# Kernel optimization log

Measured on AMD Instinct MI355X. Metric: run time of the kernel, lower is better.

Reference implementation:

```python
import jax, jax.numpy as jnp
import numpy as np

HEADS, HEAD_DIM = 8, 32
FOLD_W = FOLD_H = 8
PW = PH = 2  # proposal_w/h -> M = PW*PH centers per region


def setup_inputs() -> dict:
    key = jax.random.key(0)
    ks = jax.random.split(key, 8)
    dim, hd = 96, HEADS * HEAD_DIM
    return {
        "x": jax.random.normal(ks[0], (16, dim, 64, 64), jnp.float32),
        "Wf": jax.random.normal(ks[1], (hd, dim), jnp.float32) * 0.05,
        "bf": jax.random.normal(ks[2], (hd,), jnp.float32) * 0.01,
        "Wv": jax.random.normal(ks[3], (hd, dim), jnp.float32) * 0.05,
        "bv": jax.random.normal(ks[4], (hd,), jnp.float32) * 0.01,
        "Wp": jax.random.normal(ks[5], (dim, hd), jnp.float32) * 0.05,
        "bp": jax.random.normal(ks[6], (dim,), jnp.float32) * 0.01,
        "sim_alpha": jnp.ones((1,), jnp.float32),
        "sim_beta": jnp.zeros((1,), jnp.float32),
    }


def _l2norm(t):
    # matches torch F.normalize(dim=-1, eps=1e-12)
    n = jnp.maximum(jnp.linalg.norm(t, axis=-1, keepdims=True), 1e-12)
    return t / n


def _cluster_forward(x, Wf, bf, Wv, bv, Wp, bp, sim_alpha, sim_beta):
    B, C, W, H = x.shape
    # 1x1 convs
    v = jnp.einsum("bchw,oc->bohw", x, Wv) + bv[None, :, None, None]
    f = jnp.einsum("bchw,oc->bohw", x, Wf) + bf[None, :, None, None]

    def split_heads(t):  # b (e c) w h -> (b e) c w h
        b = t.shape[0]
        return t.reshape(b, HEADS, HEAD_DIM, W, H).reshape(b * HEADS, HEAD_DIM, W, H)

    f, v = split_heads(f), split_heads(v)

    def fold(t):  # b c (f1 w) (f2 h) -> (b f1 f2) c w h
        b, c, w0, h0 = t.shape
        ws, hs = w0 // FOLD_W, h0 // FOLD_H
        t = t.reshape(b, c, FOLD_W, ws, FOLD_H, hs)
        return t.transpose(0, 2, 4, 1, 3, 5).reshape(b * FOLD_W * FOLD_H, c, ws, hs)

    f, v = fold(f), fold(v)
    b, c, w, h = f.shape

    def pool(t):  # AdaptiveMaxPool2d((PW,PH)); divides evenly -> block max
        return t.reshape(b, c, PW, w // PW, PH, h // PH).max(axis=(3, 5))

    centers = pool(f).reshape(b, c, PW * PH).transpose(0, 2, 1)       # [b,M,c]
    value_centers = pool(v).reshape(b, c, PW * PH).transpose(0, 2, 1)  # [b,M,c]
    pts = f.reshape(b, c, w * h).transpose(0, 2, 1)                    # [b,N,c]

    cos = jnp.einsum("bmc,bnc->bmn", _l2norm(centers), _l2norm(pts))
    sim = jax.nn.sigmoid(sim_beta + sim_alpha * cos)                   # [b,M,N]

    # hard assignment: each point keeps only its best center
    idx = jnp.argmax(sim, axis=1)                                      # [b,N]
    mask = jax.nn.one_hot(idx, sim.shape[1], dtype=sim.dtype)          # [b,N,M]
    mask = jnp.transpose(mask, (0, 2, 1))                              # [b,M,N]
    sim = sim * mask

    value2 = v.reshape(b, c, w * h).transpose(0, 2, 1)                 # [b,N,c]
    # gather points -> centers
    agg = (jnp.einsum("bnc,bmn->bmc", value2, sim) + value_centers) / (
        mask.sum(axis=-1, keepdims=True) + 1.0
    )
    # dispatch centers -> points
    out = jnp.einsum("bmc,bmn->bnc", agg, sim)                         # [b,N,c]
    out = out.transpose(0, 2, 1).reshape(b, c, w, h)

    # unfold regions back
    bb = b // (FOLD_W * FOLD_H)
    out = out.reshape(bb, FOLD_W, FOLD_H, c, w, h).transpose(0, 3, 1, 4, 2, 5)
    out = out.reshape(bb, c, FOLD_W * w, FOLD_H * h)
    # merge heads: (b e) c w h -> b (e c) w h
    out = out.reshape(bb // HEADS, HEADS * HEAD_DIM, W, H)
    out = jnp.einsum("bchw,oc->bohw", out, Wp) + bp[None, :, None, None]
    return out


def reference(x, Wf, bf, Wv, bv, Wp, bp, sim_alpha, sim_beta):
    return _cluster_forward(x, Wf, bf, Wv, bv, Wp, bp, sim_alpha, sim_beta)
```

## Files before the change

kernel.cpp:

```cpp
#include <hip/hip_runtime.h>
#include <math.h>


#define TPB 256

__global__ __launch_bounds__(TPB, 4)
void cc_main(const float* __restrict__ x,
             const float* __restrict__ Wf, const float* __restrict__ bf,
             const float* __restrict__ Wv, const float* __restrict__ bv,
             const float* __restrict__ salpha, const float* __restrict__ sbeta,
             float* __restrict__ disp)
{
    __shared__ __align__(16) float smem[8320];
    __shared__ float cfs[2][132], cvs[2][132], swb[2][256], aggs[2][132];

    const int t    = threadIdx.x;
    const int lane = t & 63;
    const int wid  = __builtin_amdgcn_readfirstlane(t >> 6);
    const int tc   = t >> 4;
    const int tp   = t & 15;
    const int blk  = blockIdx.x;
    const int f1   = blk & 7;
    const int f2   = (blk >> 3) & 7;
    const int heg  = (blk >> 6) & 3;
    const int bb   = blk >> 8;
    const int fold = f1*8 + f2;

    const float* xb = x + (size_t)bb*96*4096 + (size_t)(f1*8)*64 + f2*8;

    float acc[8][4];
    {
        const float* bsrc = (tc < 8) ? (bf + heg*64 + tc*8)
                                     : (bv + heg*64 + (tc-8)*8);
        float4 b0 = *(const float4*)bsrc;
        float4 b1 = *(const float4*)(bsrc + 4);
        #pragma unroll
        for (int i = 0; i < 4; ++i) {
            acc[0][i]=b0.x; acc[1][i]=b0.y; acc[2][i]=b0.z; acc[3][i]=b0.w;
            acc[4][i]=b1.x; acc[5][i]=b1.y; acc[6][i]=b1.z; acc[7][i]=b1.w;
        }
    }

    int xoff[2], xdst[2];
    #pragma unroll
    for (int i = 0; i < 2; ++i) {
        int fl = i*256 + t;
        int kl = fl >> 4, sg = fl & 15;
        xoff[i] = kl*4096 + (sg >> 1)*64 + (sg & 1)*4;
        xdst[i] = 4096 + kl*64 + sg*4;
    }
    int wdst[4];
    const float* wptr[4];
    #pragma unroll
    for (int i = 0; i < 4; ++i) {
        int fl = i*256 + t;
        int rr = fl & 127, kq = fl >> 7;
        wptr[i] = ((rr < 64) ? (Wf + (size_t)(heg*64 + rr)*96)
                             : (Wv + (size_t)(heg*64 + rr - 64)*96)) + kq*4;
        wdst[i] = (kq*4)*128 + rr;
    }

    float4 pxr[2], pwr[4];
    #pragma unroll
    for (int i = 0; i < 2; ++i) pxr[i] = *(const float4*)(xb + xoff[i]);
    #pragma unroll
    for (int i = 0; i < 4; ++i) pwr[i] = *(const float4*)(wptr[i]);
    #pragma unroll
    for (int i = 0; i < 2; ++i) *(float4*)&smem[xdst[i]] = pxr[i];
    #pragma unroll
    for (int i = 0; i < 4; ++i) {
        smem[wdst[i]      ] = pwr[i].x;
        smem[wdst[i] + 128] = pwr[i].y;
        smem[wdst[i] + 256] = pwr[i].z;
        smem[wdst[i] + 384] = pwr[i].w;
    }
    __syncthreads();

    for (int kc = 0; ; ) {
        if (kc < 64) {
            #pragma unroll
            for (int i = 0; i < 2; ++i)
                pxr[i] = *(const float4*)(xb + (kc+32)*4096 + xoff[i]);
            #pragma unroll
            for (int i = 0; i < 4; ++i)
                pwr[i] = *(const float4*)(wptr[i] + kc + 32);
        }
        #pragma unroll 4
        for (int k = 0; k < 32; ++k) {
            float4 wa  = *(const float4*)&smem[k*128 + tc*8];
            float4 wb4 = *(const float4*)&smem[k*128 + tc*8 + 4];
            float4 xq  = *(const float4*)&smem[4096 + k*64 + tp*4];
            float xv[4] = {xq.x, xq.y, xq.z, xq.w};
            #pragma unroll
            for (int i = 0; i < 4; ++i) {
                acc[0][i] = fmaf(wa.x,  xv[i], acc[0][i]);
                acc[1][i] = fmaf(wa.y,  xv[i], acc[1][i]);
                acc[2][i] = fmaf(wa.z,  xv[i], acc[2][i]);
                acc[3][i] = fmaf(wa.w,  xv[i], acc[3][i]);
                acc[4][i] = fmaf(wb4.x, xv[i], acc[4][i]);
                acc[5][i] = fmaf(wb4.y, xv[i], acc[5][i]);
                acc[6][i] = fmaf(wb4.z, xv[i], acc[6][i]);
                acc[7][i] = fmaf(wb4.w, xv[i], acc[7][i]);
            }
        }
        if (kc == 64) break;
        __syncthreads();
        #pragma unroll
        for (int i = 0; i < 2; ++i) *(float4*)&smem[xdst[i]] = pxr[i];
        #pragma unroll
        for (int i = 0; i < 4; ++i) {
            smem[wdst[i]      ] = pwr[i].x;
            smem[wdst[i] + 128] = pwr[i].y;
            smem[wdst[i] + 256] = pwr[i].z;
            smem[wdst[i] + 384] = pwr[i].w;
        }
        __syncthreads();
        kc += 32;
    }

    const float alpha = salpha[0], beta = sbeta[0];
    __syncthreads();
    #pragma unroll
    for (int j = 0; j < 8; ++j)
        #pragma unroll
        for (int i2 = 0; i2 < 4; ++i2)
            smem[(tc*8 + j)*65 + tp*4 + i2] = acc[j][i2];
    __syncthreads();

    if (wid < 2) {
        const int he = wid, slot = he;
        {
            int m = lane >> 4, c0 = (lane & 15)*2;
            int pw = m >> 1, ph = m & 1;
            #pragma unroll
            for (int cc = 0; cc < 2; ++cc) {
                int c = c0 + cc;
                float mf = -3.402823466e38f, mv = -3.402823466e38f;
                #pragma unroll
                for (int a = 0; a < 4; ++a)
                    #pragma unroll
                    for (int b2 = 0; b2 < 4; ++b2) {
                        int n = (pw*4 + a)*8 + ph*4 + b2;
                        mf = fmaxf(mf, smem[(he*32 + c)*65 + n]);
                        mv = fmaxf(mv, smem[(64 + he*32 + c)*65 + n]);
                    }
                cfs[slot][m*33 + c] = mf;
                cvs[slot][m*33 + c] = mv;
            }
        }
        float d0=0,d1=0,d2=0,d3=0,pn=0,cn0=0,cn1=0,cn2=0,cn3=0;
        #pragma unroll 8
        for (int c = 0; c < 32; ++c) {
            float fv = smem[(he*32 + c)*65 + lane];
            float m0 = cfs[slot][c], m1 = cfs[slot][33+c];
            float m2 = cfs[slot][66+c], m3 = cfs[slot][99+c];
            d0 = fmaf(m0, fv, d0); d1 = fmaf(m1, fv, d1);
            d2 = fmaf(m2, fv, d2); d3 = fmaf(m3, fv, d3);
            pn = fmaf(fv, fv, pn);
            cn0 = fmaf(m0, m0, cn0); cn1 = fmaf(m1, m1, cn1);
            cn2 = fmaf(m2, m2, cn2); cn3 = fmaf(m3, m3, cn3);
        }
        float ip = 1.f / fmaxf(sqrtf(pn), 1e-12f);
        float z0 = beta + alpha*(d0*(1.f/fmaxf(sqrtf(cn0),1e-12f))*ip);
        float z1 = beta + alpha*(d1*(1.f/fmaxf(sqrtf(cn1),1e-12f))*ip);
        float z2 = beta + alpha*(d2*(1.f/fmaxf(sqrtf(cn2),1e-12f))*ip);
        float z3 = beta + alpha*(d3*(1.f/fmaxf(sqrtf(cn3),1e-12f))*ip);
        float s0 = 1.f/(1.f + expf(-z0));
        float s1 = 1.f/(1.f + expf(-z1));
        float s2 = 1.f/(1.f + expf(-z2));
        float s3 = 1.f/(1.f + expf(-z3));
        int bi = 0; float bvv = s0;
        if (s1 > bvv) { bvv = s1; bi = 1; }
        if (s2 > bvv) { bvv = s2; bi = 2; }
        if (s3 > bvv) { bvv = s3; bi = 3; }
        int cnt0 = __popcll(__ballot(bi == 0));
        int cnt1 = __popcll(__ballot(bi == 1));
        int cnt2 = __popcll(__ballot(bi == 2));
        int cnt3 = __popcll(__ballot(bi == 3));
        swb[slot][lane]       = (bi==0) ? bvv : 0.f;
        swb[slot][64 + lane]  = (bi==1) ? bvv : 0.f;
        swb[slot][128 + lane] = (bi==2) ? bvv : 0.f;
        swb[slot][192 + lane] = (bi==3) ? bvv : 0.f;
        #pragma unroll
        for (int it = 0; it < 2; ++it) {
            int m = it*2 + (lane >> 5);
            int c = lane & 31;
            float s = 0.f;
            #pragma unroll 8
            for (int n2 = 0; n2 < 64; ++n2)
                s = fmaf(smem[(64 + he*32 + c)*65 + n2],
                         swb[slot][m*64 + n2], s);
            int cm = (m==0) ? cnt0 : (m==1) ? cnt1 : (m==2) ? cnt2 : cnt3;
            aggs[slot][m*33 + c] = (s + cvs[slot][m*33 + c]) / (float)(cm + 1);
        }
        const int e32 = (heg*2 + he)*32;
        const size_t obase = (size_t)bb*4096 + (size_t)fold*64 + lane;
        #pragma unroll 4
        for (int c = 0; c < 32; ++c)
            disp[(size_t)(e32 + c)*65536 + obase] = aggs[slot][bi*33 + c] * bvv;
    }
}

__global__ __launch_bounds__(TPB, 8)
void cc_proj(const float* __restrict__ disp, const float* __restrict__ Wp,
             const float* __restrict__ bp, float* __restrict__ out)
{
    __shared__ __align__(16) float wch[3200];
    __shared__ __align__(16) float xch[1024];
    const int t   = threadIdx.x;
    const int toc = t >> 4;
    const int tp  = t & 15;
    const int blk = blockIdx.x;
    const int f1   = blk & 7;
    const int half = (blk >> 3) & 1;
    const int f2   = (blk >> 4) & 7;
    const int bb   = blk >> 7;
    const int fold = f1*8 + f2;
    const int pxbase = bb*4096 + fold*64 + half*32;

    float acc[6][2];
    #pragma unroll
    for (int o = 0; o < 6; ++o) {
        float b = bp[toc*6 + o];
        acc[o][0] = b; acc[o][1] = b;
    }

    int woffg[3], wdst[3];
    #pragma unroll
    for (int i = 0; i < 3; ++i) {
        int fl = i*256 + t;
        int oc2 = fl % 96, kq = fl / 96;
        woffg[i] = oc2*256 + kq*4;
        wdst[i]  = (kq*4)*100 + oc2;
    }
    const int xoffg = (t >> 3)*65536 + pxbase + (t & 7)*4;
    const int xdst  = (t >> 3)*32 + (t & 7)*4;

    float4 pwr[3], pxr;
    #pragma unroll
    for (int i = 0; i < 3; ++i) pwr[i] = *(const float4*)(Wp + woffg[i]);
    pxr = *(const float4*)(disp + xoffg);
    #pragma unroll
    for (int i = 0; i < 3; ++i) {
        wch[wdst[i]      ] = pwr[i].x; wch[wdst[i] + 100] = pwr[i].y;
        wch[wdst[i] + 200] = pwr[i].z; wch[wdst[i] + 300] = pwr[i].w;
    }
    *(float4*)&xch[xdst] = pxr;
    __syncthreads();

    for (int kc = 0; ; ) {
        if (kc < 224) {
            #pragma unroll
            for (int i = 0; i < 3; ++i)
                pwr[i] = *(const float4*)(Wp + woffg[i] + kc + 32);
            pxr = *(const float4*)(disp + xoffg + (size_t)(kc+32)*65536);
        }
        #pragma unroll 4
        for (int k = 0; k < 32; ++k) {
            float2 wA = *(const float2*)&wch[k*100 + toc*6];
            float2 wB = *(const float2*)&wch[k*100 + toc*6 + 2];
            float2 wC = *(const float2*)&wch[k*100 + toc*6 + 4];
            float2 xv = *(const float2*)&xch[k*32 + tp*2];
            acc[0][0] = fmaf(wA.x, xv.x, acc[0][0]);
            acc[0][1] = fmaf(wA.x, xv.y, acc[0][1]);
            acc[1][0] = fmaf(wA.y, xv.x, acc[1][0]);
            acc[1][1] = fmaf(wA.y, xv.y, acc[1][1]);
            acc[2][0] = fmaf(wB.x, xv.x, acc[2][0]);
            acc[2][1] = fmaf(wB.x, xv.y, acc[2][1]);
            acc[3][0] = fmaf(wB.y, xv.x, acc[3][0]);
            acc[3][1] = fmaf(wB.y, xv.y, acc[3][1]);
            acc[4][0] = fmaf(wC.x, xv.x, acc[4][0]);
            acc[4][1] = fmaf(wC.x, xv.y, acc[4][1]);
            acc[5][0] = fmaf(wC.y, xv.x, acc[5][0]);
            acc[5][1] = fmaf(wC.y, xv.y, acc[5][1]);
        }
        if (kc == 224) break;
        __syncthreads();
        #pragma unroll
        for (int i = 0; i < 3; ++i) {
            wch[wdst[i]      ] = pwr[i].x; wch[wdst[i] + 100] = pwr[i].y;
            wch[wdst[i] + 200] = pwr[i].z; wch[wdst[i] + 300] = pwr[i].w;
        }
        *(float4*)&xch[xdst] = pxr;
        __syncthreads();
        kc += 32;
    }

    const int n = half*32 + tp*2;
    const int r = n >> 3, hh = n & 7;
    size_t oaddr = (size_t)bb*96*4096 + (size_t)(toc*6)*4096
                 + (size_t)(f1*8 + r)*64 + f2*8 + hh;
    #pragma unroll
    for (int o = 0; o < 6; ++o) {
        float2 st; st.x = acc[o][0]; st.y = acc[o][1];
        *(float2*)&out[oaddr + (size_t)o*4096] = st;
    }
}

extern "C" void kernel_launch(void* const* d_in, const int* in_sizes, int n_in,
                              void* d_out, int out_size, void* d_ws, size_t ws_size,
                              hipStream_t stream) {
    (void)in_sizes; (void)n_in; (void)out_size; (void)ws_size;
    float* disp = (float*)d_ws;
    cc_main<<<dim3(4096), dim3(TPB), 0, stream>>>(
        (const float*)d_in[0],
        (const float*)d_in[1],
        (const float*)d_in[2],
        (const float*)d_in[3],
        (const float*)d_in[4],
        (const float*)d_in[7],
        (const float*)d_in[8],
        disp);
    cc_proj<<<dim3(2048), dim3(TPB), 0, stream>>>(
        disp,
        (const float*)d_in[5],
        (const float*)d_in[6],
        (float*)d_out);
}
```

Measured before the change: 260.0 us.

## Map waves to channels and pixels to lanes; read weights as uniform scalars

Both kernels are restructured so each wave owns a group of 32 (or 24) output channels and each lane owns one pixel, accumulating all channels in registers. Weights are read directly from global memory with wave-uniform addresses, which can become scalar loads, instead of being staged in LDS. The pooling max is done with DPP and a shuffle across lanes rather than through an LDS round trip. The feature projections stay in registers for the cosine step, and the projection kernel launches half as many blocks. This cuts LDS traffic and barriers, at the cost of higher register pressure and scalar-load latency.

Measured after the change: 272.1 us. 4.7% more time.

```diff
diff --git a/kernel.cpp b/kernel.cpp
--- a/kernel.cpp
+++ b/kernel.cpp
@@ -3,6 +3,13 @@
 
 
 #define TPB 256
+
+template<int CTRL>
+__device__ __forceinline__ float dpp_max(float v) {
+    int s = __builtin_bit_cast(int, v);
+    int p = __builtin_amdgcn_update_dpp(0, s, CTRL, 0xF, 0xF, true);
+    return fmaxf(v, __builtin_bit_cast(float, p));
+}
 
 __global__ __launch_bounds__(TPB, 4)
 void cc_main(const float* __restrict__ x,
@@ -11,14 +18,19 @@
              const float* __restrict__ salpha, const float* __restrict__ sbeta,
              float* __restrict__ disp)
 {
-    __shared__ __align__(16) float smem[8320];
-    __shared__ float cfs[2][132], cvs[2][132], swb[2][256], aggs[2][132];
+    __shared__ __align__(16) float xch[64*33];
+    __shared__ __align__(16) float vd[2][64*33];
+    __shared__ __align__(16) float cfs[2][128];
+    __shared__ __align__(16) float cvs[2][128];
+    __shared__ float swb[2][256];
+    __shared__ float2 bib[2][64];
+    __shared__ float cnts[2][4];
+    __shared__ float aggs[2][132];
 
     const int t    = threadIdx.x;
     const int lane = t & 63;
     const int wid  = __builtin_amdgcn_readfirstlane(t >> 6);
-    const int tc   = t >> 4;
-    const int tp   = t & 15;
+    const int he   = wid & 1;
     const int blk  = blockIdx.x;
     const int f1   = blk & 7;
     const int f2   = (blk >> 3) & 7;
@@ -28,137 +40,85 @@
 
     const float* xb = x + (size_t)bb*96*4096 + (size_t)(f1*8)*64 + f2*8;
 
-    float acc[8][4];
-    {
-        const float* bsrc = (tc < 8) ? (bf + heg*64 + tc*8)
-                                     : (bv + heg*64 + (tc-8)*8);
-        float4 b0 = *(const float4*)bsrc;
-        float4 b1 = *(const float4*)(bsrc + 4);
-        #pragma unroll
-        for (int i = 0; i < 4; ++i) {
-            acc[0][i]=b0.x; acc[1][i]=b0.y; acc[2][i]=b0.z; acc[3][i]=b0.w;
-            acc[4][i]=b1.x; acc[5][i]=b1.y; acc[6][i]=b1.z; acc[7][i]=b1.w;
-        }
-    }
-
-    int xoff[2], xdst[2];
+    const float* wrow = (wid < 2) ? (Wf + (size_t)(heg*64 + wid*32)*96)
+                                  : (Wv + (size_t)(heg*64 + (wid-2)*32)*96);
+    const float* brow = (wid < 2) ? (bf + heg*64 + wid*32)
+                                  : (bv + heg*64 + (wid-2)*32);
+
+    float acc[32];
+    #pragma unroll
+    for (int c = 0; c < 32; ++c) acc[c] = brow[c];
+
+    int xoff[2], xbs[2];
     #pragma unroll
     for (int i = 0; i < 2; ++i) {
         int fl = i*256 + t;
         int kl = fl >> 4, sg = fl & 15;
         xoff[i] = kl*4096 + (sg >> 1)*64 + (sg & 1)*4;
-        xdst[i] = 4096 + kl*64 + sg*4;
-    }
-    int wdst[4];
-    const float* wptr[4];
-    #pragma unroll
-    for (int i = 0; i < 4; ++i) {
-        int fl = i*256 + t;
-        int rr = fl & 127, kq = fl >> 7;
-        wptr[i] = ((rr < 64) ? (Wf + (size_t)(heg*64 + rr)*96)
-                             : (Wv + (size_t)(heg*64 + rr - 64)*96)) + kq*4;
-        wdst[i] = (kq*4)*128 + rr;
-    }
-
-    float4 pxr[2], pwr[4];
-    #pragma unroll
-    for (int i = 0; i < 2; ++i) pxr[i] = *(const float4*)(xb + xoff[i]);
-    #pragma unroll
-    for (int i = 0; i < 4; ++i) pwr[i] = *(const float4*)(wptr[i]);
-    #pragma unroll
-    for (int i = 0; i < 2; ++i) *(float4*)&smem[xdst[i]] = pxr[i];
-    #pragma unroll
-    for (int i = 0; i < 4; ++i) {
-        smem[wdst[i]      ] = pwr[i].x;
-        smem[wdst[i] + 128] = pwr[i].y;
-        smem[wdst[i] + 256] = pwr[i].z;
-        smem[wdst[i] + 384] = pwr[i].w;
-    }
+        xbs[i]  = ((sg >> 1)*8 + (sg & 1)*4)*33 + kl;
+    }
+
+    float4 pxr0 = *(const float4*)(xb + xoff[0]);
+    float4 pxr1 = *(const float4*)(xb + xoff[1]);
+    xch[xbs[0]] = pxr0.x; xch[xbs[0]+33] = pxr0.y;
+    xch[xbs[0]+66] = pxr0.z; xch[xbs[0]+99] = pxr0.w;
+    xch[xbs[1]] = pxr1.x; xch[xbs[1]+33] = pxr1.y;
+    xch[xbs[1]+66] = pxr1.z; xch[xbs[1]+99] = pxr1.w;
     __syncthreads();
 
+    const int lx = lane*33;
     for (int kc = 0; ; ) {
         if (kc < 64) {
-            #pragma unroll
-            for (int i = 0; i < 2; ++i)
-                pxr[i] = *(const float4*)(xb + (kc+32)*4096 + xoff[i]);
-            #pragma unroll
-            for (int i = 0; i < 4; ++i)
-                pwr[i] = *(const float4*)(wptr[i] + kc + 32);
-        }
-        #pragma unroll 4
-        for (int k = 0; k < 32; ++k) {
-            float4 wa  = *(const float4*)&smem[k*128 + tc*8];
-            float4 wb4 = *(const float4*)&smem[k*128 + tc*8 + 4];
-            float4 xq  = *(const float4*)&smem[4096 + k*64 + tp*4];
-            float xv[4] = {xq.x, xq.y, xq.z, xq.w};
-            #pragma unroll
-            for (int i = 0; i < 4; ++i) {
-                acc[0][i] = fmaf(wa.x,  xv[i], acc[0][i]);
-                acc[1][i] = fmaf(wa.y,  xv[i], acc[1][i]);
-                acc[2][i] = fmaf(wa.z,  xv[i], acc[2][i]);
-                acc[3][i] = fmaf(wa.w,  xv[i], acc[3][i]);
-                acc[4][i] = fmaf(wb4.x, xv[i], acc[4][i]);
-                acc[5][i] = fmaf(wb4.y, xv[i], acc[5][i]);
-                acc[6][i] = fmaf(wb4.z, xv[i], acc[6][i]);
-                acc[7][i] = fmaf(wb4.w, xv[i], acc[7][i]);
+            pxr0 = *(const float4*)(xb + (kc+32)*4096 + xoff[0]);
+            pxr1 = *(const float4*)(xb + (kc+32)*4096 + xoff[1]);
+        }
+        #pragma unroll
+        for (int kg = 0; kg < 4; ++kg) {
+            float xv[8];
+            #pragma unroll
+            for (int j = 0; j < 8; ++j) xv[j] = xch[lx + kg*8 + j];
+            #pragma unroll
+            for (int c = 0; c < 32; ++c) {
+                const float* wp = wrow + c*96 + (kc + kg*8);
+                #pragma unroll
+                for (int j = 0; j < 8; ++j)
+                    acc[c] = fmaf(wp[j], xv[j], acc[c]);
             }
         }
         if (kc == 64) break;
         __syncthreads();
-        #pragma unroll
-        for (int i = 0; i < 2; ++i) *(float4*)&smem[xdst[i]] = pxr[i];
-        #pragma unroll
-        for (int i = 0; i < 4; ++i) {
-            smem[wdst[i]      ] = pwr[i].x;
-            smem[wdst[i] + 128] = pwr[i].y;
-            smem[wdst[i] + 256] = pwr[i].z;
-            smem[wdst[i] + 384] = pwr[i].w;
-        }
+        xch[xbs[0]] = pxr0.x; xch[xbs[0]+33] = pxr0.y;
+        xch[xbs[0]+66] = pxr0.z; xch[xbs[0]+99] = pxr0.w;
+        xch[xbs[1]] = pxr1.x; xch[xbs[1]+33] = pxr1.y;
+        xch[xbs[1]+66] = pxr1.z; xch[xbs[1]+99] = pxr1.w;
         __syncthreads();
         kc += 32;
     }
 
     const float alpha = salpha[0], beta = sbeta[0];
-    __syncthreads();
-    #pragma unroll
-    for (int j = 0; j < 8; ++j)
-        #pragma unroll
-        for (int i2 = 0; i2 < 4; ++i2)
-            smem[(tc*8 + j)*65 + tp*4 + i2] = acc[j][i2];
-    __syncthreads();
+    const int m = ((lane >> 5) & 1)*2 + ((lane >> 2) & 1);
+    const bool rep = (lane & 27) == 0;
+    #pragma unroll
+    for (int c = 0; c < 32; ++c) {
+        float rm = acc[c];
+        rm = dpp_max<0xB1>(rm);
+        rm = dpp_max<0x4E>(rm);
+        rm = dpp_max<0x128>(rm);
+        rm = fmaxf(rm, __shfl_xor(rm, 16));
+        if (rep) { if (wid < 2) cfs[he][c*4 + m] = rm; else cvs[he][c*4 + m] = rm; }
+    }
 
     if (wid < 2) {
-        const int he = wid, slot = he;
-        {
-            int m = lane >> 4, c0 = (lane & 15)*2;
-            int pw = m >> 1, ph = m & 1;
-            #pragma unroll
-            for (int cc = 0; cc < 2; ++cc) {
-                int c = c0 + cc;
-                float mf = -3.402823466e38f, mv = -3.402823466e38f;
-                #pragma unroll
-                for (int a = 0; a < 4; ++a)
-                    #pragma unroll
-                    for (int b2 = 0; b2 < 4; ++b2) {
-                        int n = (pw*4 + a)*8 + ph*4 + b2;
-                        mf = fmaxf(mf, smem[(he*32 + c)*65 + n]);
-                        mv = fmaxf(mv, smem[(64 + he*32 + c)*65 + n]);
-                    }
-                cfs[slot][m*33 + c] = mf;
-                cvs[slot][m*33 + c] = mv;
-            }
-        }
         float d0=0,d1=0,d2=0,d3=0,pn=0,cn0=0,cn1=0,cn2=0,cn3=0;
-        #pragma unroll 8
+        #pragma unroll
         for (int c = 0; c < 32; ++c) {
-            float fv = smem[(he*32 + c)*65 + lane];
-            float m0 = cfs[slot][c], m1 = cfs[slot][33+c];
-            float m2 = cfs[slot][66+c], m3 = cfs[slot][99+c];
-            d0 = fmaf(m0, fv, d0); d1 = fmaf(m1, fv, d1);
-            d2 = fmaf(m2, fv, d2); d3 = fmaf(m3, fv, d3);
+            float4 cf = *(const float4*)&cfs[he][c*4];
+            float fv = acc[c];
+            d0 = fmaf(cf.x, fv, d0); d1 = fmaf(cf.y, fv, d1);
+            d2 = fmaf(cf.z, fv, d2); d3 = fmaf(cf.w, fv, d3);
             pn = fmaf(fv, fv, pn);
-            cn0 = fmaf(m0, m0, cn0); cn1 = fmaf(m1, m1, cn1);
-            cn2 = fmaf(m2, m2, cn2); cn3 = fmaf(m3, m3, cn3);
+            cn0 = fmaf(cf.x, cf.x, cn0); cn1 = fmaf(cf.y, cf.y, cn1);
+            cn2 = fmaf(cf.z, cf.z, cn2); cn3 = fmaf(cf.w, cf.w, cn3);
         }
         float ip = 1.f / fmaxf(sqrtf(pn), 1e-12f);
         float z0 = beta + alpha*(d0*(1.f/fmaxf(sqrtf(cn0),1e-12f))*ip);
@@ -177,124 +137,113 @@
         int cnt1 = __popcll(__ballot(bi == 1));
         int cnt2 = __popcll(__ballot(bi == 2));
         int cnt3 = __popcll(__ballot(bi == 3));
-        swb[slot][lane]       = (bi==0) ? bvv : 0.f;
-        swb[slot][64 + lane]  = (bi==1) ? bvv : 0.f;
-        swb[slot][128 + lane] = (bi==2) ? bvv : 0.f;
-        swb[slot][192 + lane] = (bi==3) ? bvv : 0.f;
+        swb[he][lane]       = (bi==0) ? bvv : 0.f;
+        swb[he][64 + lane]  = (bi==1) ? bvv : 0.f;
+        swb[he][128 + lane] = (bi==2) ? bvv : 0.f;
+        swb[he][192 + lane] = (bi==3) ? bvv : 0.f;
+        bib[he][lane] = make_float2(bvv, (float)bi);
+        if (lane == 0) {
+            cnts[he][0] = (float)cnt0; cnts[he][1] = (float)cnt1;
+            cnts[he][2] = (float)cnt2; cnts[he][3] = (float)cnt3;
+        }
+    } else {
+        #pragma unroll
+        for (int c = 0; c < 32; ++c) vd[he][lane*33 + c] = acc[c];
+    }
+    __syncthreads();
+
+    if (wid >= 2) {
+        const int cI = lane & 31;
         #pragma unroll
         for (int it = 0; it < 2; ++it) {
-            int m = it*2 + (lane >> 5);
-            int c = lane & 31;
+            int mm = it*2 + (lane >> 5);
             float s = 0.f;
             #pragma unroll 8
             for (int n2 = 0; n2 < 64; ++n2)
-                s = fmaf(smem[(64 + he*32 + c)*65 + n2],
-                         swb[slot][m*64 + n2], s);
-            int cm = (m==0) ? cnt0 : (m==1) ? cnt1 : (m==2) ? cnt2 : cnt3;
-            aggs[slot][m*33 + c] = (s + cvs[slot][m*33 + c]) / (float)(cm + 1);
-        }
+                s = fmaf(vd[he][n2*33 + cI], swb[he][mm*64 + n2], s);
+            aggs[he][mm*33 + cI] = (s + cvs[he][cI*4 + mm]) / (cnts[he][mm] + 1.f);
+        }
+        float2 b2 = bib[he][lane];
+        float bvv = b2.x; int bi = (int)b2.y;
         const int e32 = (heg*2 + he)*32;
         const size_t obase = (size_t)bb*4096 + (size_t)fold*64 + lane;
         #pragma unroll 4
         for (int c = 0; c < 32; ++c)
-            disp[(size_t)(e32 + c)*65536 + obase] = aggs[slot][bi*33 + c] * bvv;
-    }
-}
-
-__global__ __launch_bounds__(TPB, 8)
+            disp[(size_t)(e32 + c)*65536 + obase] = aggs[he][bi*33 + c] * bvv;
+    }
+}
+
+__global__ __launch_bounds__(TPB, 4)
 void cc_proj(const float* __restrict__ disp, const float* __restrict__ Wp,
              const float* __restrict__ bp, float* __restrict__ out)
 {
-    __shared__ __align__(16) float wch[3200];
-    __shared__ __align__(16) float xch[1024];
-    const int t   = threadIdx.x;
-    const int toc = t >> 4;
-    const int tp  = t & 15;
-    const int blk = blockIdx.x;
+    __shared__ __align__(16) float xch[64*33];
+    const int t    = threadIdx.x;
+    const int lane = t & 63;
+    const int wid  = __builtin_amdgcn_readfirstlane(t >> 6);
+    const int blk  = blockIdx.x;
     const int f1   = blk & 7;
-    const int half = (blk >> 3) & 1;
-    const int f2   = (blk >> 4) & 7;
-    const int bb   = blk >> 7;
+    const int f2   = (blk >> 3) & 7;
+    const int bb   = blk >> 6;
     const int fold = f1*8 + f2;
-    const int pxbase = bb*4096 + fold*64 + half*32;
-
-    float acc[6][2];
-    #pragma unroll
-    for (int o = 0; o < 6; ++o) {
-        float b = bp[toc*6 + o];
-        acc[o][0] = b; acc[o][1] = b;
-    }
-
-    int woffg[3], wdst[3];
-    #pragma unroll
-    for (int i = 0; i < 3; ++i) {
+    const int pxbase = bb*4096 + fold*64;
+
+    const float* wrow = Wp + (size_t)(wid*24)*256;
+    float acc[24];
+    #pragma unroll
+    for (int o = 0; o < 24; ++o) acc[o] = bp[wid*24 + o];
+
+    int xoff[2], xbs[2];
+    #pragma unroll
+    for (int i = 0; i < 2; ++i) {
         int fl = i*256 + t;
-        int oc2 = fl % 96, kq = fl / 96;
-        woffg[i] = oc2*256 + kq*4;
-        wdst[i]  = (kq*4)*100 + oc2;
-    }
-    const int xoffg = (t >> 3)*65536 + pxbase + (t & 7)*4;
-    const int xdst  = (t >> 3)*32 + (t & 7)*4;
-
-    float4 pwr[3], pxr;
-    #pragma unroll
-    for (int i = 0; i < 3; ++i) pwr[i] = *(const float4*)(Wp + woffg[i]);
-    pxr = *(const float4*)(disp + xoffg);
-    #pragma unroll
-    for (int i = 0; i < 3; ++i) {
-        wch[wdst[i]      ] = pwr[i].x; wch[wdst[i] + 100] = pwr[i].y;
-        wch[wdst[i] + 200] = pwr[i].z; wch[wdst[i] + 300] = pwr[i].w;
-    }
-    *(float4*)&xch[xdst] = pxr;
+        int kl = fl >> 4, sg = fl & 15;
+        xoff[i] = kl*65536 + pxbase + sg*4;
+        xbs[i]  = (sg*4)*33 + kl;
+    }
+
+    float4 pxr0 = *(const float4*)(disp + xoff[0]);
+    float4 pxr1 = *(const float4*)(disp + xoff[1]);
+    xch[xbs[0]] = pxr0.x; xch[xbs[0]+33] = pxr0.y;
+    xch[xbs[0]+66] = pxr0.z; xch[xbs[0]+99] = pxr0.w;
+    xch[xbs[1]] = pxr1.x; xch[xbs[1]+33] = pxr1.y;
+    xch[xbs[1]+66] = pxr1.z; xch[xbs[1]+99] = pxr1.w;
     __syncthreads();
 
+    const int lx = lane*33;
     for (int kc = 0; ; ) {
         if (kc < 224) {
-            #pragma unroll
-            for (int i = 0; i < 3; ++i)
-                pwr[i] = *(const float4*)(Wp + woffg[i] + kc + 32);
-            pxr = *(const float4*)(disp + xoffg + (size_t)(kc+32)*65536);
-        }
-        #pragma unroll 4
-        for (int k = 0; k < 32; ++k) {
-            float2 wA = *(const float2*)&wch[k*100 + toc*6];
-            float2 wB = *(const float2*)&wch[k*100 + toc*6 + 2];
-            float2 wC = *(const float2*)&wch[k*100 + toc*6 + 4];
-            float2 xv = *(const float2*)&xch[k*32 + tp*2];
-            acc[0][0] = fmaf(wA.x, xv.x, acc[0][0]);
-            acc[0][1] = fmaf(wA.x, xv.y, acc[0][1]);
-            acc[1][0] = fmaf(wA.y, xv.x, acc[1][0]);
-            acc[1][1] = fmaf(wA.y, xv.y, acc[1][1]);
-            acc[2][0] = fmaf(wB.x, xv.x, acc[2][0]);
-            acc[2][1] = fmaf(wB.x, xv.y, acc[2][1]);
-            acc[3][0] = fmaf(wB.y, xv.x, acc[3][0]);
-            acc[3][1] = fmaf(wB.y, xv.y, acc[3][1]);
-            acc[4][0] = fmaf(wC.x, xv.x, acc[4][0]);
-            acc[4][1] = fmaf(wC.x, xv.y, acc[4][1]);
-            acc[5][0] = fmaf(wC.y, xv.x, acc[5][0]);
-            acc[5][1] = fmaf(wC.y, xv.y, acc[5][1]);
+            pxr0 = *(const float4*)(disp + (size_t)(kc+32)*65536 + xoff[0] - (size_t)0);
+            pxr1 = *(const float4*)(disp + (size_t)(kc+32)*65536 + xoff[1] - (size_t)0);
+        }
+        #pragma unroll
+        for (int kg = 0; kg < 4; ++kg) {
+            float xv[8];
+            #pragma unroll
+            for (int j = 0; j < 8; ++j) xv[j] = xch[lx + kg*8 + j];
+            #pragma unroll
+            for (int o = 0; o < 24; ++o) {
+                const float* wp = wrow + o*256 + (kc + kg*8);
+                #pragma unroll
+                for (int j = 0; j < 8; ++j)
+                    acc[o] = fmaf(wp[j], xv[j], acc[o]);
+            }
         }
         if (kc == 224) break;
         __syncthreads();
-        #pragma unroll
-        for (int i = 0; i < 3; ++i) {
-            wch[wdst[i]      ] = pwr[i].x; wch[wdst[i] + 100] = pwr[i].y;
-            wch[wdst[i] + 200] = pwr[i].z; wch[wdst[i] + 300] = pwr[i].w;
-        }
-        *(float4*)&xch[xdst] = pxr;
+        xch[xbs[0]] = pxr0.x; xch[xbs[0]+33] = pxr0.y;
+        xch[xbs[0]+66] = pxr0.z; xch[xbs[0]+99] = pxr0.w;
+        xch[xbs[1]] = pxr1.x; xch[xbs[1]+33] = pxr1.y;
+        xch[xbs[1]+66] = pxr1.z; xch[xbs[1]+99] = pxr1.w;
         __syncthreads();
         kc += 32;
     }
 
-    const int n = half*32 + tp*2;
-    const int r = n >> 3, hh = n & 7;
-    size_t oaddr = (size_t)bb*96*4096 + (size_t)(toc*6)*4096
-                 + (size_t)(f1*8 + r)*64 + f2*8 + hh;
-    #pragma unroll
-    for (int o = 0; o < 6; ++o) {
-        float2 st; st.x = acc[o][0]; st.y = acc[o][1];
-        *(float2*)&out[oaddr + (size_t)o*4096] = st;
-    }
+    const int r = lane >> 3, hh = lane & 7;
+    const size_t ob = (size_t)bb*96*4096 + (size_t)(f1*8 + r)*64 + f2*8 + hh;
+    #pragma unroll
+    for (int o = 0; o < 24; ++o)
+        out[ob + (size_t)(wid*24 + o)*4096] = acc[o];
 }
 
 extern "C" void kernel_launch(void* const* d_in, const int* in_sizes, int n_in,
@@ -311,7 +260,7 @@
         (const float*)d_in[7],
         (const float*)d_in[8],
         disp);
-    cc_proj<<<dim3(2048), dim3(TPB), 0, stream>>>(
+    cc_proj<<<dim3(1024), dim3(TPB), 0, stream>>>(
         disp,
         (const float*)d_in[5],
         (const float*)d_in[6],
```

## Enlarge projection register tile and offload aggregation to idle waves in main kernel

Applied to the files above, without the earlier changes.

The projection kernel now gives each of 192 threads an 8x4 output tile covering a full 64-pixel fold, with float4 shared loads and stores. This raises arithmetic intensity and halves the block count. In the main kernel, the per-head aggregation and dispatch stage is handed to waves 2-3 after a barrier, with best values, indices and counts passed through shared memory, so that work is spread across more waves. In exchange it adds an extra __syncthreads and changes occupancy for cc_proj.

After: 248.2 us. -4.5%, faster.

```diff
diff --git a/kernel.cpp b/kernel.cpp
--- a/kernel.cpp
+++ b/kernel.cpp
@@ -13,6 +13,8 @@
 {
     __shared__ __align__(16) float smem[8320];
     __shared__ float cfs[2][132], cvs[2][132], swb[2][256], aggs[2][132];
+    __shared__ float2 bib[2][64];
+    __shared__ float cnts[2][4];
 
     const int t    = threadIdx.x;
     const int lane = t & 63;
@@ -181,18 +183,30 @@
         swb[slot][64 + lane]  = (bi==1) ? bvv : 0.f;
         swb[slot][128 + lane] = (bi==2) ? bvv : 0.f;
         swb[slot][192 + lane] = (bi==3) ? bvv : 0.f;
+        bib[slot][lane] = make_float2(bvv, (float)bi);
+        if (lane == 0) {
+            cnts[slot][0] = (float)cnt0; cnts[slot][1] = (float)cnt1;
+            cnts[slot][2] = (float)cnt2; cnts[slot][3] = (float)cnt3;
+        }
+    }
+    __syncthreads();
+
+    if (wid >= 2) {
+        const int he = wid - 2, slot = he;
+        const int cI = lane & 31;
         #pragma unroll
         for (int it = 0; it < 2; ++it) {
-            int m = it*2 + (lane >> 5);
-            int c = lane & 31;
+            int mm = it*2 + (lane >> 5);
             float s = 0.f;
             #pragma unroll 8
             for (int n2 = 0; n2 < 64; ++n2)
-                s = fmaf(smem[(64 + he*32 + c)*65 + n2],
-                         swb[slot][m*64 + n2], s);
-            int cm = (m==0) ? cnt0 : (m==1) ? cnt1 : (m==2) ? cnt2 : cnt3;
-            aggs[slot][m*33 + c] = (s + cvs[slot][m*33 + c]) / (float)(cm + 1);
-        }
+                s = fmaf(smem[(64 + he*32 + cI)*65 + n2],
+                         swb[slot][mm*64 + n2], s);
+            aggs[slot][mm*33 + cI] = (s + cvs[slot][mm*33 + cI])
+                                   / (cnts[slot][mm] + 1.f);
+        }
+        float2 b2 = bib[slot][lane];
+        float bvv = b2.x; int bi = (int)b2.y;
         const int e32 = (heg*2 + he)*32;
         const size_t obase = (size_t)bb*4096 + (size_t)fold*64 + lane;
         #pragma unroll 4
@@ -201,99 +215,108 @@
     }
 }
 
-__global__ __launch_bounds__(TPB, 8)
+__global__ __launch_bounds__(192, 3)
 void cc_proj(const float* __restrict__ disp, const float* __restrict__ Wp,
              const float* __restrict__ bp, float* __restrict__ out)
 {
     __shared__ __align__(16) float wch[3200];
-    __shared__ __align__(16) float xch[1024];
+    __shared__ __align__(16) float xch[2048];
     const int t   = threadIdx.x;
-    const int toc = t >> 4;
-    const int tp  = t & 15;
+    const int cg  = t >> 4;
+    const int pg  = t & 15;
     const int blk = blockIdx.x;
-    const int f1   = blk & 7;
-    const int half = (blk >> 3) & 1;
-    const int f2   = (blk >> 4) & 7;
-    const int bb   = blk >> 7;
-    const int fold = f1*8 + f2;
-    const int pxbase = bb*4096 + fold*64 + half*32;
-
-    float acc[6][2];
-    #pragma unroll
-    for (int o = 0; o < 6; ++o) {
-        float b = bp[toc*6 + o];
-        acc[o][0] = b; acc[o][1] = b;
-    }
-
-    int woffg[3], wdst[3];
+    const int f1  = blk & 7;
+    const int f2  = (blk >> 3) & 7;
+    const int bb  = blk >> 6;
+    const int pxbase = bb*4096 + (f1*8 + f2)*64;
+
+    float acc[8][4];
+    {
+        const float* bsrc = bp + cg*8;
+        float4 b0 = *(const float4*)bsrc, b1 = *(const float4*)(bsrc + 4);
+        float bj[8] = {b0.x,b0.y,b0.z,b0.w,b1.x,b1.y,b1.z,b1.w};
+        #pragma unroll
+        for (int j = 0; j < 8; ++j)
+            #pragma unroll
+            for (int i = 0; i < 4; ++i) acc[j][i] = bj[j];
+    }
+
+    int wdst[4]; int woff[4];
+    #pragma unroll
+    for (int i = 0; i < 4; ++i) {
+        int fl = i*192 + t;
+        int rr = fl % 96, kq = fl / 96;
+        woff[i] = rr*256 + kq*4;
+        wdst[i] = (kq*4)*100 + rr;
+    }
+    int xdst[3]; int xoff[3];
     #pragma unroll
     for (int i = 0; i < 3; ++i) {
-        int fl = i*256 + t;
-        int oc2 = fl % 96, kq = fl / 96;
-        woffg[i] = oc2*256 + kq*4;
-        wdst[i]  = (kq*4)*100 + oc2;
-    }
-    const int xoffg = (t >> 3)*65536 + pxbase + (t & 7)*4;
-    const int xdst  = (t >> 3)*32 + (t & 7)*4;
-
-    float4 pwr[3], pxr;
-    #pragma unroll
-    for (int i = 0; i < 3; ++i) pwr[i] = *(const float4*)(Wp + woffg[i]);
-    pxr = *(const float4*)(disp + xoffg);
-    #pragma unroll
-    for (int i = 0; i < 3; ++i) {
+        int fl = i*192 + t;
+        int kl = fl >> 4, p4 = (fl & 15)*4;
+        xoff[i] = kl*65536 + pxbase + p4;
+        xdst[i] = kl*64 + p4;
+    }
+    const bool x3 = (t < 128);
+
+    float4 pwr[4], pxr[3];
+    #pragma unroll
+    for (int i = 0; i < 4; ++i) pwr[i] = *(const float4*)(Wp + woff[i]);
+    pxr[0] = *(const float4*)(disp + xoff[0]);
+    pxr[1] = *(const float4*)(disp + xoff[1]);
+    if (x3) pxr[2] = *(const float4*)(disp + xoff[2]);
+    #pragma unroll
+    for (int i = 0; i < 4; ++i) {
         wch[wdst[i]      ] = pwr[i].x; wch[wdst[i] + 100] = pwr[i].y;
         wch[wdst[i] + 200] = pwr[i].z; wch[wdst[i] + 300] = pwr[i].w;
     }
-    *(float4*)&xch[xdst] = pxr;
+    *(float4*)&xch[xdst[0]] = pxr[0];
+    *(float4*)&xch[xdst[1]] = pxr[1];
+    if (x3) *(float4*)&xch[xdst[2]] = pxr[2];
     __syncthreads();
 
     for (int kc = 0; ; ) {
         if (kc < 224) {
             #pragma unroll
-            for (int i = 0; i < 3; ++i)
-                pwr[i] = *(const float4*)(Wp + woffg[i] + kc + 32);
-            pxr = *(const float4*)(disp + xoffg + (size_t)(kc+32)*65536);
+            for (int i = 0; i < 4; ++i)
+                pwr[i] = *(const float4*)(Wp + woff[i] + kc + 32);
+            pxr[0] = *(const float4*)(disp + xoff[0] + (size_t)(kc+32)*65536);
+            pxr[1] = *(const float4*)(disp + xoff[1] + (size_t)(kc+32)*65536);
+            if (x3) pxr[2] = *(const float4*)(disp + xoff[2] + (size_t)(kc+32)*65536);
         }
         #pragma unroll 4
         for (int k = 0; k < 32; ++k) {
-            float2 wA = *(const float2*)&wch[k*100 + toc*6];
-            float2 wB = *(const float2*)&wch[k*100 + toc*6 + 2];
-            float2 wC = *(const float2*)&wch[k*100 + toc*6 + 4];
-            float2 xv = *(const float2*)&xch[k*32 + tp*2];
-            acc[0][0] = fmaf(wA.x, xv.x, acc[0][0]);
-            acc[0][1] = fmaf(wA.x, xv.y, acc[0][1]);
-            acc[1][0] = fmaf(wA.y, xv.x, acc[1][0]);
-            acc[1][1] = fmaf(wA.y, xv.y, acc[1][1]);
-            acc[2][0] = fmaf(wB.x, xv.x, acc[2][0]);
-            acc[2][1] = fmaf(wB.x, xv.y, acc[2][1]);
-            acc[3][0] = fmaf(wB.y, xv.x, acc[3][0]);
-            acc[3][1] = fmaf(wB.y, xv.y, acc[3][1]);
-            acc[4][0] = fmaf(wC.x, xv.x, acc[4][0]);
-            acc[4][1] = fmaf(wC.x, xv.y, acc[4][1]);
-            acc[5][0] = fmaf(wC.y, xv.x, acc[5][0]);
-            acc[5][1] = fmaf(wC.y, xv.y, acc[5][1]);
+            float4 wa = *(const float4*)&wch[k*100 + cg*8];
+            float4 wb = *(const float4*)&wch[k*100 + cg*8 + 4];
+            float4 xq = *(const float4*)&xch[k*64 + pg*4];
+            float wv[8] = {wa.x,wa.y,wa.z,wa.w,wb.x,wb.y,wb.z,wb.w};
+            float xv[4] = {xq.x,xq.y,xq.z,xq.w};
+            #pragma unroll
+            for (int j = 0; j < 8; ++j)
+                #pragma unroll
+                for (int i = 0; i < 4; ++i)
+                    acc[j][i] = fmaf(wv[j], xv[i], acc[j][i]);
         }
         if (kc == 224) break;
         __syncthreads();
         #pragma unroll
-        for (int i = 0; i < 3; ++i) {
+        for (int i = 0; i < 4; ++i) {
             wch[wdst[i]      ] = pwr[i].x; wch[wdst[i] + 100] = pwr[i].y;
             wch[wdst[i] + 200] = pwr[i].z; wch[wdst[i] + 300] = pwr[i].w;
         }
-        *(float4*)&xch[xdst] = pxr;
+        *(float4*)&xch[xdst[0]] = pxr[0];
+        *(float4*)&xch[xdst[1]] = pxr[1];
+        if (x3) *(float4*)&xch[xdst[2]] = pxr[2];
         __syncthreads();
         kc += 32;
     }
 
-    const int n = half*32 + tp*2;
-    const int r = n >> 3, hh = n & 7;
-    size_t oaddr = (size_t)bb*96*4096 + (size_t)(toc*6)*4096
-                 + (size_t)(f1*8 + r)*64 + f2*8 + hh;
-    #pragma unroll
-    for (int o = 0; o < 6; ++o) {
-        float2 st; st.x = acc[o][0]; st.y = acc[o][1];
-        *(float2*)&out[oaddr + (size_t)o*4096] = st;
+    const size_t ob = (size_t)bb*96*4096 + (size_t)(f1*8 + (pg >> 1))*64
+                    + f2*8 + (pg & 1)*4;
+    #pragma unroll
+    for (int j = 0; j < 8; ++j) {
+        float4 st = make_float4(acc[j][0], acc[j][1], acc[j][2], acc[j][3]);
+        *(float4*)&out[ob + (size_t)(cg*8 + j)*4096] = st;
     }
 }
 
@@ -311,7 +334,7 @@
         (const float*)d_in[7],
         (const float*)d_in[8],
         disp);
-    cc_proj<<<dim3(2048), dim3(TPB), 0, stream>>>(
+    cc_proj<<<dim3(1024), dim3(192), 0, stream>>>(
         disp,
         (const float*)d_in[5],
         (const float*)d_in[6],
```
